# Kernel optimization log

Measured on AMD Instinct MI355X. Metric: run time of the kernel, lower is better.

The kernel has to match this reference:

```python
import jax, jax.numpy as jnp
import numpy as np

BN_EPS = 1e-5

def _bn_relu(x, gamma, beta):
    # training-mode BatchNorm1d: biased batch stats over (B, N) per channel
    mean = x.mean(axis=(0, 2), keepdims=True)
    var = x.var(axis=(0, 2), keepdims=True)
    xn = (x - mean) * jax.lax.rsqrt(var + BN_EPS)
    return jax.nn.relu(xn * gamma[None, :, None] + beta[None, :, None])


def setup_inputs() -> dict:
    key = jax.random.key(0)
    ks = jax.random.split(key, 12)
    B, n1, n2, c1, c2 = 16, 4096, 1024, 128, 256
    in_ch, mlp = c1 + c2, [256, 128]
    xyz1 = jax.random.uniform(ks[0], (B, n1, 3), dtype=jnp.float32)
    xyz2 = jax.random.uniform(ks[1], (B, n2, 3), dtype=jnp.float32)
    feat1 = jax.random.normal(ks[2], (B, c1, n1), dtype=jnp.float32)
    feat2 = jax.random.normal(ks[3], (B, c2, n2), dtype=jnp.float32)
    # Conv1d(k=1) weights as (out, in) matrices; kaiming-ish scale
    w0 = jax.random.normal(ks[4], (mlp[0], in_ch), dtype=jnp.float32) / np.sqrt(in_ch)
    b0 = jnp.zeros((mlp[0],), jnp.float32)
    g0 = jnp.ones((mlp[0],), jnp.float32)
    be0 = jnp.zeros((mlp[0],), jnp.float32)
    w1 = jax.random.normal(ks[5], (mlp[1], mlp[0]), dtype=jnp.float32) / np.sqrt(mlp[0])
    b1 = jnp.zeros((mlp[1],), jnp.float32)
    g1 = jnp.ones((mlp[1],), jnp.float32)
    be1 = jnp.zeros((mlp[1],), jnp.float32)
    return {"xyz1": xyz1, "xyz2": xyz2, "feat1": feat1, "feat2": feat2,
            "w0": w0, "b0": b0, "g0": g0, "be0": be0,
            "w1": w1, "b1": b1, "g1": g1, "be1": be1}


def reference(xyz1, xyz2, feat1, feat2, w0, b0, g0, be0, w1, b1, g1, be1):
    # three_nn_interpolate: squared pairwise dists (B, n1, n2)
    d = jnp.sum((xyz1[:, :, None, :] - xyz2[:, None, :, :]) ** 2, axis=-1)
    neg_d3, idx3 = jax.lax.top_k(-d, 3)          # 3 smallest dists
    d3 = -neg_d3                                  # (B, n1, 3)
    w = 1.0 / (d3 + 1e-8)
    w = w / jnp.sum(w, axis=-1, keepdims=True)
    # gather feat2 at knn indices: (B, c2, n1, 3)
    gathered = jnp.take_along_axis(feat2[:, :, None, :], idx3[:, None, :, :], axis=3)
    interp = jnp.sum(gathered * w[:, None, :, :], axis=-1)  # (B, c2, n1)

    x = jnp.concatenate([feat1, interp], axis=1)            # (B, c1+c2, n1)
    x = _bn_relu(jnp.einsum('oc,bcn->bon', w0, x) + b0[None, :, None], g0, be0)
    x = _bn_relu(jnp.einsum('oc,bcn->bon', w1, x) + b1[None, :, None], g1, be1)
    return x
```

## Files before the change

kernel.cpp:

```cpp
#include <hip/hip_runtime.h>
#include <hip/hip_bf16.h>

typedef unsigned short u16;
typedef __attribute__((ext_vector_type(8))) __bf16 bf16x8;
typedef __attribute__((ext_vector_type(4))) float floatx4;

#define B_   16
#define N1_  4096
#define N2_  1024
#define C1_  128
#define C2_  256
#define CIN_ 384
#define CM_  256
#define CO_  128

__device__ __forceinline__ u16 f2bf(float f) {
  unsigned u = __float_as_uint(f);
  u = (u + 0x7fffu + ((u >> 16) & 1u)) >> 16;
  return (u16)u;
}
__device__ __forceinline__ float bf2f(u16 h) {
  return __uint_as_float(((unsigned)h) << 16);
}

union U128 { uint4 u; bf16x8 v; u16 s[8]; };

__device__ __forceinline__ bf16x8 ldfrag(const u16* p) {
  U128 x; x.u = *(const uint4*)p; return x.v;
}
__device__ __forceinline__ uint4 pack8(const u16* h) {
  uint4 u;
  u.x = (unsigned)h[0] | ((unsigned)h[1] << 16);
  u.y = (unsigned)h[2] | ((unsigned)h[3] << 16);
  u.z = (unsigned)h[4] | ((unsigned)h[5] << 16);
  u.w = (unsigned)h[6] | ((unsigned)h[7] << 16);
  return u;
}


__global__ __launch_bounds__(256) void knn_part_kernel(
    const float* __restrict__ xyz1, const float* __restrict__ xyz2,
    float* __restrict__ pd, int* __restrict__ pi,
    const float* __restrict__ w0, const float* __restrict__ w1,
    u16* __restrict__ w0b, u16* __restrict__ w1b)
{
  __shared__ float4 sp[128];
  int t = threadIdx.x;
  if (blockIdx.x == 16) {
    int item = (blockIdx.y * 8 + blockIdx.z) * 256 + t;
    if (item < 12288) {
      int m = item / 48, kc = item % 48;
      const float* p = w0 + m * CIN_ + kc * 8;
      u16 h8[8];
      #pragma unroll
      for (int j = 0; j < 8; ++j) h8[j] = f2bf(p[j]);
      int mt = m >> 4, col = m & 15, kt = kc >> 2, quad = kc & 3;
      *(uint4*)(w0b + ((mt*12 + kt)*512 + (quad*16 + col)*8)) = pack8(h8);
    } else if (item < 16384) {
      int i2 = item - 12288;
      int m = i2 >> 5, kc = i2 & 31;
      const float* p = w1 + m * CM_ + kc * 8;
      u16 h8[8];
      #pragma unroll
      for (int j = 0; j < 8; ++j) h8[j] = f2bf(p[j]);
      int mt = m >> 4, col = m & 15, kt = kc >> 2, quad = kc & 3;
      *(uint4*)(w1b + ((mt*8 + kt)*512 + (quad*16 + col)*8)) = pack8(h8);
    }
    return;
  }
  int b = blockIdx.y, chunk = blockIdx.z;
  const float* p2 = xyz2 + ((size_t)b * N2_ + chunk * 128) * 3;
  if (t < 128) sp[t] = make_float4(p2[t*3], p2[t*3+1], p2[t*3+2], 0.f);
  __syncthreads();
  int i = blockIdx.x * 256 + t;
  const float* p1 = xyz1 + ((size_t)b * N1_ + i) * 3;
  float x = p1[0], y = p1[1], z = p1[2];
  float d0 = 1e30f, d1 = 1e30f, d2 = 1e30f;
  int i0 = 0, i1 = 0, i2 = 0;
  int jb = chunk * 128;
  #pragma unroll 4
  for (int j = 0; j < 128; ++j) {
    float4 p = sp[j];
    float dx = x - p.x, dy = y - p.y, dz = z - p.z;
    float d = dx*dx + dy*dy + dz*dz;
    int jj = jb + j;
    bool c2 = d < d2, c1 = d < d1, c0 = d < d0;
    d2 = c1 ? d1 : (c2 ? d  : d2);
    i2 = c1 ? i1 : (c2 ? jj : i2);
    d1 = c0 ? d0 : (c1 ? d  : d1);
    i1 = c0 ? i0 : (c1 ? jj : i1);
    d0 = c0 ? d  : d0;
    i0 = c0 ? jj : i0;
  }
  int o = chunk*65536 + b*4096 + i;
  pd[o] = d0; pd[o + 524288] = d1; pd[o + 1048576] = d2;
  pi[o] = i0; pi[o + 524288] = i1; pi[o + 1048576] = i2;
}

__global__ __launch_bounds__(256) void knn_merge_kernel(
    const float* __restrict__ pd, const int* __restrict__ pi,
    int* __restrict__ idx_out, float* __restrict__ w_out)
{
  int p = blockIdx.x * 256 + threadIdx.x;
  float d0 = 1e30f, d1 = 1e30f, d2 = 1e30f;
  int i0 = 0, i1 = 0, i2 = 0;
  #pragma unroll
  for (int c = 0; c < 8; ++c) {
    int o = c*65536 + p;
    #pragma unroll
    for (int k = 0; k < 3; ++k) {
      float d = pd[o + k*524288];
      int ix = pi[o + k*524288];
      bool c2 = d < d2, c1 = d < d1, c0 = d < d0;
      d2 = c1 ? d1 : (c2 ? d  : d2);
      i2 = c1 ? i1 : (c2 ? ix : i2);
      d1 = c0 ? d0 : (c1 ? d  : d1);
      i1 = c0 ? i0 : (c1 ? ix : i1);
      d0 = c0 ? d  : d0;
      i0 = c0 ? ix : i0;
    }
  }
  float w0 = 1.f/(d0+1e-8f), w1 = 1.f/(d1+1e-8f), w2 = 1.f/(d2+1e-8f);
  float inv = 1.f/(w0+w1+w2);
  idx_out[p]          = i0;
  idx_out[p +  65536] = i1;
  idx_out[p + 131072] = i2;
  w_out[p]            = w0*inv;
  w_out[p +  65536]   = w1*inv;
  w_out[p + 131072]   = w2*inv;
}

__global__ __launch_bounds__(256) void tr2_kernel(
    const float* __restrict__ feat2, u16* __restrict__ feat2Tb)
{
  __shared__ float sA[64][257];
  int b = blockIdx.y;
  int n0 = blockIdx.x * 64;
  int t = threadIdx.x;
  #pragma unroll
  for (int j = 0; j < 16; ++j) {
    int flat4 = t + j * 256;
    int c = flat4 >> 4, nn4 = (flat4 & 15) * 4;
    float4 v = *(const float4*)(feat2 + ((size_t)b*C2_ + c)*N2_ + n0 + nn4);
    sA[nn4+0][c] = v.x; sA[nn4+1][c] = v.y; sA[nn4+2][c] = v.z; sA[nn4+3][c] = v.w;
  }
  __syncthreads();
  int nn = t & 63, chunk = t >> 6;
  u16* dst = feat2Tb + ((size_t)b*N2_ + n0 + nn)*C2_ + chunk*64;
  #pragma unroll
  for (int g = 0; g < 8; ++g) {
    u16 h8[8];
    #pragma unroll
    for (int j = 0; j < 8; ++j) h8[j] = f2bf(sA[nn][chunk*64 + g*8 + j]);
    *(uint4*)(dst + g*8) = pack8(h8);
  }
}

__global__ __launch_bounds__(256) void prep_fused_kernel(
    const float* __restrict__ feat1, const u16* __restrict__ feat2Tb,
    const int* __restrict__ idx_in, const float* __restrict__ w_in,
    u16* __restrict__ xcatT)
{
  __shared__ float sA[64][133];
  int b = blockIdx.y;
  int t = threadIdx.x;
  if (blockIdx.x < 64) {
    int n0 = blockIdx.x * 64;
    #pragma unroll
    for (int j = 0; j < 8; ++j) {
      int flat4 = t + j * 256;
      int c = flat4 >> 4, nn4 = (flat4 & 15) * 4;
      float4 v = *(const float4*)(feat1 + ((size_t)b*C1_ + c)*N1_ + n0 + nn4);
      sA[nn4+0][c] = v.x; sA[nn4+1][c] = v.y; sA[nn4+2][c] = v.z; sA[nn4+3][c] = v.w;
    }
    __syncthreads();
    int nn = t & 63, chunk = t >> 6;
    int n = n0 + nn, nt = n >> 4, col = n & 15;
    u16* tb = xcatT + ((size_t)b*256 + nt)*12*512;
    #pragma unroll
    for (int g = 0; g < 4; ++g) {
      int c0 = chunk*32 + g*8;
      u16 h8[8];
      #pragma unroll
      for (int j = 0; j < 8; ++j) h8[j] = f2bf(sA[nn][c0 + j]);
      *(uint4*)(tb + (size_t)chunk*512 + (g*16 + col)*8) = pack8(h8);
    }
  } else {
    int p0 = (blockIdx.x - 64) * 64;
    int seg = t & 31;
    int pl  = t >> 5;
    #pragma unroll 2
    for (int pass = 0; pass < 8; ++pass) {
      int n = p0 + pass*8 + pl;
      int base = b*N1_ + n;
      int i0 = idx_in[base], i1 = idx_in[base + 65536], i2 = idx_in[base + 131072];
      float w0 = w_in[base], w1 = w_in[base + 65536], w2 = w_in[base + 131072];
      const u16* fb = feat2Tb + (size_t)b*N2_*C2_ + seg*8;
      U128 a, c, d;
      a.u = *(const uint4*)(fb + (size_t)i0*C2_);
      c.u = *(const uint4*)(fb + (size_t)i1*C2_);
      d.u = *(const uint4*)(fb + (size_t)i2*C2_);
      u16 h8[8];
      #pragma unroll
      for (int j = 0; j < 8; ++j)
        h8[j] = f2bf(w0*bf2f(a.s[j]) + w1*bf2f(c.s[j]) + w2*bf2f(d.s[j]));
      int nt = n >> 4, col = n & 15;
      int kt = 4 + (seg >> 2), quad = seg & 3;
      *(uint4*)(xcatT + (((size_t)b*256 + nt)*12 + kt)*512 + (quad*16 + col)*8) = pack8(h8);
    }
  }
}

__global__ __launch_bounds__(256) void gemm1_mfma(
    const u16* __restrict__ xcatT, const u16* __restrict__ w0b,
    const float* __restrict__ b0p, u16* __restrict__ y0T,
    float* __restrict__ p0)
{
  __shared__ u16 sbuf[2][16][512];
  __shared__ float ps[4][64][2];
  int t = threadIdx.x;
  int wave = t >> 6, lane = t & 63;
  int col = lane & 15, quad = lane >> 4;
  int wm = wave >> 1, wn = wave & 1;
  int b = blockIdx.y;
  int mtb8 = blockIdx.z * 8;
  int ntb8 = blockIdx.x * 8;

  const u16* asrc = w0b + (size_t)mtb8 * 12 * 512 + lane * 8;
  const u16* bsrc = xcatT + ((size_t)(b * 256 + ntb8) * 12) * 512 + lane * 8;
  const u16* stage_base = (wave < 2) ? (asrc + (size_t)(wave * 4) * 12 * 512)
                                     : (bsrc + (size_t)((wave - 2) * 4) * 12 * 512);

  floatx4 acc[4][4] = {};

  #pragma unroll
  for (int i = 0; i < 4; ++i)
    __builtin_amdgcn_global_load_lds(
        (const __attribute__((address_space(1))) void*)(stage_base + (size_t)i * 12 * 512),
        (__attribute__((address_space(3))) void*)(&sbuf[0][wave * 4 + i][0]),
        16, 0, 0);
  __syncthreads();

  int cur = 0;
  #pragma unroll 1
  for (int kt = 0; kt < 12; ++kt) {
    if (kt < 11) {
      #pragma unroll
      for (int i = 0; i < 4; ++i)
        __builtin_amdgcn_global_load_lds(
            (const __attribute__((address_space(1))) void*)(stage_base + (size_t)(i * 12 + kt + 1) * 512),
            (__attribute__((address_space(3))) void*)(&sbuf[cur ^ 1][wave * 4 + i][0]),
            16, 0, 0);
    }
    bf16x8 af[4], bfr[4];
    #pragma unroll
    for (int i = 0; i < 4; ++i) {
      af[i]  = ldfrag(&sbuf[cur][wm * 4 + i][lane * 8]);
      bfr[i] = ldfrag(&sbuf[cur][8 + wn * 4 + i][lane * 8]);
    }
    #pragma unroll
    for (int mt = 0; mt < 4; ++mt)
      #pragma unroll
      for (int nt = 0; nt < 4; ++nt)
        acc[mt][nt] = __builtin_amdgcn_mfma_f32_16x16x32_bf16(af[mt], bfr[nt], acc[mt][nt], 0, 0, 0);
    __syncthreads();
    cur ^= 1;
  }

  int m0 = blockIdx.z*128 + wm*64;
  #pragma unroll
  for (int mt = 0; mt < 4; ++mt) {
    float4 bias4 = *(const float4*)(b0p + m0 + mt*16 + quad*4);
    float bia[4] = {bias4.x, bias4.y, bias4.z, bias4.w};
    int kt_out = (m0 >> 5) + (mt >> 1);
    int quad_out = ((mt & 1) << 1) | (quad >> 1);
    int j0 = (quad & 1) * 4;
    float s[4] = {}, q[4] = {};
    int ntb = ntb8 + wn*4;
    #pragma unroll
    for (int nt = 0; nt < 4; ++nt) {
      int nt_g = ntb + nt;
      u16 h[4];
      #pragma unroll
      for (int r = 0; r < 4; ++r) {
        float v = acc[mt][nt][r] + bia[r];
        u16 hh = f2bf(v);
        float vr = bf2f(hh);
        h[r] = hh; s[r] += vr; q[r] += vr*vr;
      }
      *(ushort4*)(y0T + (((size_t)b*256 + nt_g)*8 + kt_out)*512 + (quad_out*16 + col)*8 + j0)
          = make_ushort4(h[0], h[1], h[2], h[3]);
    }
    #pragma unroll
    for (int r = 0; r < 4; ++r) {
      float ss = s[r], qq = q[r];
      #pragma unroll
      for (int msk = 1; msk < 16; msk <<= 1) { ss += __shfl_xor(ss, msk); qq += __shfl_xor(qq, msk); }
      if (col == 0) {
        ps[wave][mt*16 + quad*4 + r][0] = ss;
        ps[wave][mt*16 + quad*4 + r][1] = qq;
      }
    }
  }
  __syncthreads();
  {
    int c = t >> 1, k = t & 1;
    int wbase = (c >> 6) * 2, ch = c & 63;
    float v = ps[wbase][ch][k] + ps[wbase+1][ch][k];
    size_t l = (size_t)blockIdx.z*512 + blockIdx.y*32 + blockIdx.x;
    p0[l*256 + t] = v;
  }
}

__global__ __launch_bounds__(256) void stats_kernel(
    const float* __restrict__ p, const float* __restrict__ g,
    const float* __restrict__ be, float* __restrict__ scale,
    float* __restrict__ shift, int half_split)
{
  int c = blockIdx.x, t = threadIdx.x;
  size_t base = half_split ? ((size_t)(c >> 7) * 512 * 256 + (size_t)(c & 127) * 2)
                           : ((size_t)c * 2);
  float s = 0.f, q = 0.f;
  #pragma unroll
  for (int i = 0; i < 2; ++i) {
    float2 v = *(const float2*)(p + base + (size_t)(t + i*256) * 256);
    s += v.x; q += v.y;
  }
  #pragma unroll
  for (int m = 1; m < 64; m <<= 1) { s += __shfl_xor(s, m); q += __shfl_xor(q, m); }
  __shared__ float2 red[4];
  if ((t & 63) == 0) red[t >> 6] = make_float2(s, q);
  __syncthreads();
  if (t == 0) {
    float ss = red[0].x + red[1].x + red[2].x + red[3].x;
    float qq = red[0].y + red[1].y + red[2].y + red[3].y;
    float mu  = ss * (1.f/65536.f);
    float var = qq * (1.f/65536.f) - mu*mu;
    float a = g[c] * rsqrtf(var + 1e-5f);
    scale[c] = a; shift[c] = be[c] - mu*a;
  }
}

__global__ __launch_bounds__(256) void gemm2_mfma(
    const u16* __restrict__ y0T, const u16* __restrict__ w1b,
    const float* __restrict__ b1p,
    const float* __restrict__ scale0, const float* __restrict__ shift0,
    float* __restrict__ out, float* __restrict__ p1)
{
  __shared__ float a0s[CM_], bb0s[CM_];
  __shared__ float ps[4][64][2];
  int t = threadIdx.x;
  a0s[t] = scale0[t]; bb0s[t] = shift0[t];
  __syncthreads();
  int wave = t >> 6, lane = t & 63;
  int col = lane & 15, quad = lane >> 4;
  int wm = wave >> 1, wn = wave & 1;
  int b = blockIdx.y;
  int mtb = wm*4;
  int ntb = blockIdx.x*8 + wn*4;

  const u16* ap = w1b + lane*8;
  const u16* bp = y0T + ((size_t)(b*256 + ntb)*8)*512 + lane*8;

  floatx4 acc[4][4] = {};
  bf16x8 af[4], afn[4];
  U128 braw[4], brawn[4];
  #pragma unroll
  for (int i = 0; i < 4; ++i) {
    af[i] = ldfrag(ap + (size_t)((mtb+i)*8)*512);
    braw[i].u = *(const uint4*)(bp + (size_t)(i*8)*512);
  }
  #pragma unroll 1
  for (int kt = 1; kt < 8; ++kt) {
    #pragma unroll
    for (int i = 0; i < 4; ++i) afn[i] = ldfrag(ap + (size_t)((mtb+i)*8 + kt)*512);
    #pragma unroll
    for (int i = 0; i < 4; ++i) brawn[i].u = *(const uint4*)(bp + (size_t)(i*8 + kt)*512);
    int c0 = (kt-1)*32 + quad*8;
    float4 av0 = *(const float4*)&a0s[c0], av1 = *(const float4*)&a0s[c0+4];
    float4 bv0 = *(const float4*)&bb0s[c0], bv1 = *(const float4*)&bb0s[c0+4];
    float av[8] = {av0.x,av0.y,av0.z,av0.w,av1.x,av1.y,av1.z,av1.w};
    float bv[8] = {bv0.x,bv0.y,bv0.z,bv0.w,bv1.x,bv1.y,bv1.z,bv1.w};
    bf16x8 bfv[4];
    #pragma unroll
    for (int i = 0; i < 4; ++i) {
      u16 h8[8];
      #pragma unroll
      for (int j = 0; j < 8; ++j)
        h8[j] = f2bf(fmaxf(fmaf(bf2f(braw[i].s[j]), av[j], bv[j]), 0.f));
      U128 x; x.u = pack8(h8); bfv[i] = x.v;
    }
    #pragma unroll
    for (int mt = 0; mt < 4; ++mt)
      #pragma unroll
      for (int nt = 0; nt < 4; ++nt)
        acc[mt][nt] = __builtin_amdgcn_mfma_f32_16x16x32_bf16(af[mt], bfv[nt], acc[mt][nt], 0, 0, 0);
    #pragma unroll
    for (int i = 0; i < 4; ++i) { af[i] = afn[i]; braw[i] = brawn[i]; }
  }
  {
    int c0 = 7*32 + quad*8;
    float4 av0 = *(const float4*)&a0s[c0], av1 = *(const float4*)&a0s[c0+4];
    float4 bv0 = *(const float4*)&bb0s[c0], bv1 = *(const float4*)&bb0s[c0+4];
    float av[8] = {av0.x,av0.y,av0.z,av0.w,av1.x,av1.y,av1.z,av1.w};
    float bv[8] = {bv0.x,bv0.y,bv0.z,bv0.w,bv1.x,bv1.y,bv1.z,bv1.w};
    bf16x8 bfv[4];
    #pragma unroll
    for (int i = 0; i < 4; ++i) {
      u16 h8[8];
      #pragma unroll
      for (int j = 0; j < 8; ++j)
        h8[j] = f2bf(fmaxf(fmaf(bf2f(braw[i].s[j]), av[j], bv[j]), 0.f));
      U128 x; x.u = pack8(h8); bfv[i] = x.v;
    }
    #pragma unroll
    for (int mt = 0; mt < 4; ++mt)
      #pragma unroll
      for (int nt = 0; nt < 4; ++nt)
        acc[mt][nt] = __builtin_amdgcn_mfma_f32_16x16x32_bf16(af[mt], bfv[nt], acc[mt][nt], 0, 0, 0);
  }

  int m0 = wm*64;
  int n0 = blockIdx.x*128 + wn*64;
  #pragma unroll
  for (int mt = 0; mt < 4; ++mt) {
    float4 bias4 = *(const float4*)(b1p + m0 + mt*16 + quad*4);
    float bia[4] = {bias4.x, bias4.y, bias4.z, bias4.w};
    float s[4] = {}, q[4] = {};
    #pragma unroll
    for (int nt = 0; nt < 4; ++nt) {
      int n = n0 + nt*16 + col;
      #pragma unroll
      for (int r = 0; r < 4; ++r) {
        float v = acc[mt][nt][r] + bia[r];
        out[((size_t)b*CO_ + m0 + mt*16 + quad*4 + r)*N1_ + n] = v;
        s[r] += v; q[r] += v*v;
      }
    }
    #pragma unroll
    for (int r = 0; r < 4; ++r) {
      float ss = s[r], qq = q[r];
      #pragma unroll
      for (int msk = 1; msk < 16; msk <<= 1) { ss += __shfl_xor(ss, msk); qq += __shfl_xor(qq, msk); }
      if (col == 0) {
        ps[wave][mt*16 + quad*4 + r][0] = ss;
        ps[wave][mt*16 + quad*4 + r][1] = qq;
      }
    }
  }
  __syncthreads();
  {
    int c = t >> 1, k = t & 1;
    int wbase = (c >> 6) * 2, ch = c & 63;
    float v = ps[wbase][ch][k] + ps[wbase+1][ch][k];
    size_t l = (size_t)blockIdx.y*32 + blockIdx.x;
    p1[l*256 + t] = v;
  }
}

__global__ __launch_bounds__(256) void bnrelu_kernel(
    float* __restrict__ out, const float* __restrict__ scale1, const float* __restrict__ shift1)
{
  int idx = blockIdx.x * 256 + threadIdx.x;
  int c = (idx >> 10) & (CO_ - 1);
  float a = scale1[c];
  float bb = shift1[c];
  float4 v = ((const float4*)out)[idx];
  v.x = fmaxf(fmaf(v.x, a, bb), 0.f);
  v.y = fmaxf(fmaf(v.y, a, bb), 0.f);
  v.z = fmaxf(fmaf(v.z, a, bb), 0.f);
  v.w = fmaxf(fmaf(v.w, a, bb), 0.f);
  ((float4*)out)[idx] = v;
}

extern "C" void kernel_launch(void* const* d_in, const int* in_sizes, int n_in,
                              void* d_out, int out_size, void* d_ws, size_t ws_size,
                              hipStream_t stream)
{
  const float* xyz1  = (const float*)d_in[0];
  const float* xyz2  = (const float*)d_in[1];
  const float* feat1 = (const float*)d_in[2];
  const float* feat2 = (const float*)d_in[3];
  const float* w0    = (const float*)d_in[4];
  const float* b0    = (const float*)d_in[5];
  const float* g0    = (const float*)d_in[6];
  const float* be0   = (const float*)d_in[7];
  const float* w1    = (const float*)d_in[8];
  const float* b1    = (const float*)d_in[9];
  const float* g1    = (const float*)d_in[10];
  const float* be1   = (const float*)d_in[11];
  float* out = (float*)d_out;
  char* ws = (char*)d_ws;

  u16*   xcatT   = (u16*)ws;
  float* knn_pd  = (float*)ws;
  int*   knn_pi  = (int*)(ws + 6291456);
  u16*   y0T     = (u16*)(ws + 50331648);
  u16*   feat2Tb = (u16*)(ws + 50331648);
  u16*   w0b     = (u16*)(ws + 83886080);
  u16*   w1b     = (u16*)(ws + 84082688);
  int*   idx_buf = (int*)(ws + 84148224);
  float* w_buf   = (float*)(ws + 84934656);
  float* p0      = (float*)(ws + 85721088);
  float* p1      = (float*)(ws + 86769664);
  float* scale0  = (float*)(ws + 87293952);
  float* shift0  = scale0 + 256;
  float* scale1  = scale0 + 512;
  float* shift1  = scale0 + 640;

  knn_part_kernel <<<dim3(17,16,8),   256, 0, stream>>>(xyz1, xyz2, knn_pd, knn_pi, w0, w1, w0b, w1b);
  knn_merge_kernel<<<256,             256, 0, stream>>>(knn_pd, knn_pi, idx_buf, w_buf);
  tr2_kernel      <<<dim3(16,16),     256, 0, stream>>>(feat2, feat2Tb);
  prep_fused_kernel<<<dim3(128,16),   256, 0, stream>>>(feat1, feat2Tb, idx_buf, w_buf, xcatT);
  gemm1_mfma      <<<dim3(32,16,2),   256, 0, stream>>>(xcatT, w0b, b0, y0T, p0);
  stats_kernel    <<<256,             256, 0, stream>>>(p0, g0, be0, scale0, shift0, 1);
  gemm2_mfma      <<<dim3(32,16),     256, 0, stream>>>(y0T, w1b, b1, scale0, shift0, out, p1);
  stats_kernel    <<<128,             256, 0, stream>>>(p1, g1, be1, scale1, shift1, 0);
  bnrelu_kernel   <<<8192,            256, 0, stream>>>(out, scale1, shift1);
}
```

Before: 244.7 us.

## Fuse kNN merge with feat2 transpose, branch top-3 insert, LDS-staged gemm2

The kNN inner loop now uses an early-out branch, so the top-3 insertion only runs when a candidate beats the current third-best. The merge and feat2 transpose kernels become one launch that splits blocks by blockIdx.x, saving a launch. gemm2 is rewritten to stage weight and activation fragments into double-buffered LDS with global_load_lds, using smaller 64-column tiles and twice as many blocks for occupancy. The stats kernel takes a loop count to match, and the p1 partials move into the reused workspace region at offset 0.

```diff
diff --git a/kernel.cpp b/kernel.cpp
--- a/kernel.cpp
+++ b/kernel.cpp
@@ -83,60 +83,57 @@
     float4 p = sp[j];
     float dx = x - p.x, dy = y - p.y, dz = z - p.z;
     float d = dx*dx + dy*dy + dz*dz;
-    int jj = jb + j;
-    bool c2 = d < d2, c1 = d < d1, c0 = d < d0;
-    d2 = c1 ? d1 : (c2 ? d  : d2);
-    i2 = c1 ? i1 : (c2 ? jj : i2);
-    d1 = c0 ? d0 : (c1 ? d  : d1);
-    i1 = c0 ? i0 : (c1 ? jj : i1);
-    d0 = c0 ? d  : d0;
-    i0 = c0 ? jj : i0;
+    if (d < d2) {
+      int jj = jb + j;
+      if (d < d0)      { d2=d1; i2=i1; d1=d0; i1=i0; d0=d; i0=jj; }
+      else if (d < d1) { d2=d1; i2=i1; d1=d;  i1=jj; }
+      else             { d2=d;  i2=jj; }
+    }
   }
   int o = chunk*65536 + b*4096 + i;
   pd[o] = d0; pd[o + 524288] = d1; pd[o + 1048576] = d2;
   pi[o] = i0; pi[o + 524288] = i1; pi[o + 1048576] = i2;
 }
 
-__global__ __launch_bounds__(256) void knn_merge_kernel(
+__global__ __launch_bounds__(256) void tr2m_kernel(
+    const float* __restrict__ feat2, u16* __restrict__ feat2Tb,
     const float* __restrict__ pd, const int* __restrict__ pi,
     int* __restrict__ idx_out, float* __restrict__ w_out)
 {
-  int p = blockIdx.x * 256 + threadIdx.x;
-  float d0 = 1e30f, d1 = 1e30f, d2 = 1e30f;
-  int i0 = 0, i1 = 0, i2 = 0;
-  #pragma unroll
-  for (int c = 0; c < 8; ++c) {
-    int o = c*65536 + p;
-    #pragma unroll
-    for (int k = 0; k < 3; ++k) {
-      float d = pd[o + k*524288];
-      int ix = pi[o + k*524288];
-      bool c2 = d < d2, c1 = d < d1, c0 = d < d0;
-      d2 = c1 ? d1 : (c2 ? d  : d2);
-      i2 = c1 ? i1 : (c2 ? ix : i2);
-      d1 = c0 ? d0 : (c1 ? d  : d1);
-      i1 = c0 ? i0 : (c1 ? ix : i1);
-      d0 = c0 ? d  : d0;
-      i0 = c0 ? ix : i0;
-    }
-  }
-  float w0 = 1.f/(d0+1e-8f), w1 = 1.f/(d1+1e-8f), w2 = 1.f/(d2+1e-8f);
-  float inv = 1.f/(w0+w1+w2);
-  idx_out[p]          = i0;
-  idx_out[p +  65536] = i1;
-  idx_out[p + 131072] = i2;
-  w_out[p]            = w0*inv;
-  w_out[p +  65536]   = w1*inv;
-  w_out[p + 131072]   = w2*inv;
-}
-
-__global__ __launch_bounds__(256) void tr2_kernel(
-    const float* __restrict__ feat2, u16* __restrict__ feat2Tb)
-{
   __shared__ float sA[64][257];
+  int t = threadIdx.x;
+  if (blockIdx.x >= 16) {
+    int p = (blockIdx.y * 16 + (blockIdx.x - 16)) * 256 + t;
+    float d0 = 1e30f, d1 = 1e30f, d2 = 1e30f;
+    int i0 = 0, i1 = 0, i2 = 0;
+    #pragma unroll
+    for (int c = 0; c < 8; ++c) {
+      int o = c*65536 + p;
+      #pragma unroll
+      for (int k = 0; k < 3; ++k) {
+        float d = pd[o + k*524288];
+        int ix = pi[o + k*524288];
+        bool c2 = d < d2, c1 = d < d1, c0 = d < d0;
+        d2 = c1 ? d1 : (c2 ? d  : d2);
+        i2 = c1 ? i1 : (c2 ? ix : i2);
+        d1 = c0 ? d0 : (c1 ? d  : d1);
+        i1 = c0 ? i0 : (c1 ? ix : i1);
+        d0 = c0 ? d  : d0;
+        i0 = c0 ? ix : i0;
+      }
+    }
+    float w0 = 1.f/(d0+1e-8f), w1 = 1.f/(d1+1e-8f), w2 = 1.f/(d2+1e-8f);
+    float inv = 1.f/(w0+w1+w2);
+    idx_out[p]          = i0;
+    idx_out[p +  65536] = i1;
+    idx_out[p + 131072] = i2;
+    w_out[p]            = w0*inv;
+    w_out[p +  65536]   = w1*inv;
+    w_out[p + 131072]   = w2*inv;
+    return;
+  }
   int b = blockIdx.y;
   int n0 = blockIdx.x * 64;
-  int t = threadIdx.x;
   #pragma unroll
   for (int j = 0; j < 16; ++j) {
     int flat4 = t + j * 256;
@@ -315,14 +312,13 @@
 __global__ __launch_bounds__(256) void stats_kernel(
     const float* __restrict__ p, const float* __restrict__ g,
     const float* __restrict__ be, float* __restrict__ scale,
-    float* __restrict__ shift, int half_split)
+    float* __restrict__ shift, int half_split, int nl)
 {
   int c = blockIdx.x, t = threadIdx.x;
   size_t base = half_split ? ((size_t)(c >> 7) * 512 * 256 + (size_t)(c & 127) * 2)
                            : ((size_t)c * 2);
   float s = 0.f, q = 0.f;
-  #pragma unroll
-  for (int i = 0; i < 2; ++i) {
+  for (int i = 0; i < nl; ++i) {
     float2 v = *(const float2*)(p + base + (size_t)(t + i*256) * 256);
     s += v.x; q += v.y;
   }
@@ -347,88 +343,82 @@
     const float* __restrict__ scale0, const float* __restrict__ shift0,
     float* __restrict__ out, float* __restrict__ p1)
 {
+  __shared__ u16 sbuf[2][12][512];
   __shared__ float a0s[CM_], bb0s[CM_];
   __shared__ float ps[4][64][2];
   int t = threadIdx.x;
   a0s[t] = scale0[t]; bb0s[t] = shift0[t];
-  __syncthreads();
   int wave = t >> 6, lane = t & 63;
   int col = lane & 15, quad = lane >> 4;
   int wm = wave >> 1, wn = wave & 1;
   int b = blockIdx.y;
-  int mtb = wm*4;
-  int ntb = blockIdx.x*8 + wn*4;
-
-  const u16* ap = w1b + lane*8;
-  const u16* bp = y0T + ((size_t)(b*256 + ntb)*8)*512 + lane*8;
-
-  floatx4 acc[4][4] = {};
-  bf16x8 af[4], afn[4];
-  U128 braw[4], brawn[4];
-  #pragma unroll
-  for (int i = 0; i < 4; ++i) {
-    af[i] = ldfrag(ap + (size_t)((mtb+i)*8)*512);
-    braw[i].u = *(const uint4*)(bp + (size_t)(i*8)*512);
-  }
+  int ntb4 = blockIdx.x * 4;
+
+  const u16* src[3];
+  #pragma unroll
+  for (int i = 0; i < 3; ++i) {
+    int f = wave * 3 + i;
+    src[i] = (f < 8) ? (w1b + (size_t)(f * 8) * 512 + lane * 8)
+                     : (y0T + ((size_t)(b * 256 + ntb4 + (f - 8)) * 8) * 512 + lane * 8);
+  }
+
+  floatx4 acc[4][2] = {};
+
+  #pragma unroll
+  for (int i = 0; i < 3; ++i)
+    __builtin_amdgcn_global_load_lds(
+        (const __attribute__((address_space(1))) void*)(src[i]),
+        (__attribute__((address_space(3))) void*)(&sbuf[0][wave * 3 + i][0]),
+        16, 0, 0);
+  __syncthreads();
+
+  int cur = 0;
   #pragma unroll 1
-  for (int kt = 1; kt < 8; ++kt) {
-    #pragma unroll
-    for (int i = 0; i < 4; ++i) afn[i] = ldfrag(ap + (size_t)((mtb+i)*8 + kt)*512);
-    #pragma unroll
-    for (int i = 0; i < 4; ++i) brawn[i].u = *(const uint4*)(bp + (size_t)(i*8 + kt)*512);
-    int c0 = (kt-1)*32 + quad*8;
-    float4 av0 = *(const float4*)&a0s[c0], av1 = *(const float4*)&a0s[c0+4];
-    float4 bv0 = *(const float4*)&bb0s[c0], bv1 = *(const float4*)&bb0s[c0+4];
-    float av[8] = {av0.x,av0.y,av0.z,av0.w,av1.x,av1.y,av1.z,av1.w};
-    float bv[8] = {bv0.x,bv0.y,bv0.z,bv0.w,bv1.x,bv1.y,bv1.z,bv1.w};
-    bf16x8 bfv[4];
-    #pragma unroll
-    for (int i = 0; i < 4; ++i) {
+  for (int kt = 0; kt < 8; ++kt) {
+    if (kt < 7) {
+      #pragma unroll
+      for (int i = 0; i < 3; ++i)
+        __builtin_amdgcn_global_load_lds(
+            (const __attribute__((address_space(1))) void*)(src[i] + (size_t)(kt + 1) * 512),
+            (__attribute__((address_space(3))) void*)(&sbuf[cur ^ 1][wave * 3 + i][0]),
+            16, 0, 0);
+    }
+    bf16x8 af[4]; U128 braw[2];
+    #pragma unroll
+    for (int i = 0; i < 4; ++i) af[i] = ldfrag(&sbuf[cur][wm * 4 + i][lane * 8]);
+    #pragma unroll
+    for (int j = 0; j < 2; ++j) braw[j].u = *(const uint4*)(&sbuf[cur][8 + wn * 2 + j][lane * 8]);
+    int c0 = kt * 32 + quad * 8;
+    float av[8], bv[8];
+    *(float4*)&av[0] = *(const float4*)&a0s[c0];  *(float4*)&av[4] = *(const float4*)&a0s[c0+4];
+    *(float4*)&bv[0] = *(const float4*)&bb0s[c0]; *(float4*)&bv[4] = *(const float4*)&bb0s[c0+4];
+    bf16x8 bfv[2];
+    #pragma unroll
+    for (int j = 0; j < 2; ++j) {
       u16 h8[8];
       #pragma unroll
-      for (int j = 0; j < 8; ++j)
-        h8[j] = f2bf(fmaxf(fmaf(bf2f(braw[i].s[j]), av[j], bv[j]), 0.f));
-      U128 x; x.u = pack8(h8); bfv[i] = x.v;
+      for (int e = 0; e < 8; ++e)
+        h8[e] = f2bf(fmaxf(fmaf(bf2f(braw[j].s[e]), av[e], bv[e]), 0.f));
+      U128 x; x.u = pack8(h8); bfv[j] = x.v;
     }
     #pragma unroll
     for (int mt = 0; mt < 4; ++mt)
       #pragma unroll
-      for (int nt = 0; nt < 4; ++nt)
+      for (int nt = 0; nt < 2; ++nt)
         acc[mt][nt] = __builtin_amdgcn_mfma_f32_16x16x32_bf16(af[mt], bfv[nt], acc[mt][nt], 0, 0, 0);
-    #pragma unroll
-    for (int i = 0; i < 4; ++i) { af[i] = afn[i]; braw[i] = brawn[i]; }
-  }
-  {
-    int c0 = 7*32 + quad*8;
-    float4 av0 = *(const float4*)&a0s[c0], av1 = *(const float4*)&a0s[c0+4];
-    float4 bv0 = *(const float4*)&bb0s[c0], bv1 = *(const float4*)&bb0s[c0+4];
-    float av[8] = {av0.x,av0.y,av0.z,av0.w,av1.x,av1.y,av1.z,av1.w};
-    float bv[8] = {bv0.x,bv0.y,bv0.z,bv0.w,bv1.x,bv1.y,bv1.z,bv1.w};
-    bf16x8 bfv[4];
-    #pragma unroll
-    for (int i = 0; i < 4; ++i) {
-      u16 h8[8];
-      #pragma unroll
-      for (int j = 0; j < 8; ++j)
-        h8[j] = f2bf(fmaxf(fmaf(bf2f(braw[i].s[j]), av[j], bv[j]), 0.f));
-      U128 x; x.u = pack8(h8); bfv[i] = x.v;
-    }
-    #pragma unroll
-    for (int mt = 0; mt < 4; ++mt)
-      #pragma unroll
-      for (int nt = 0; nt < 4; ++nt)
-        acc[mt][nt] = __builtin_amdgcn_mfma_f32_16x16x32_bf16(af[mt], bfv[nt], acc[mt][nt], 0, 0, 0);
-  }
-
-  int m0 = wm*64;
-  int n0 = blockIdx.x*128 + wn*64;
+    __syncthreads();
+    cur ^= 1;
+  }
+
+  int m0 = wm * 64;
+  int n0 = blockIdx.x * 64 + wn * 32;
   #pragma unroll
   for (int mt = 0; mt < 4; ++mt) {
     float4 bias4 = *(const float4*)(b1p + m0 + mt*16 + quad*4);
     float bia[4] = {bias4.x, bias4.y, bias4.z, bias4.w};
     float s[4] = {}, q[4] = {};
     #pragma unroll
-    for (int nt = 0; nt < 4; ++nt) {
+    for (int nt = 0; nt < 2; ++nt) {
       int n = n0 + nt*16 + col;
       #pragma unroll
       for (int r = 0; r < 4; ++r) {
@@ -453,7 +443,7 @@
     int c = t >> 1, k = t & 1;
     int wbase = (c >> 6) * 2, ch = c & 63;
     float v = ps[wbase][ch][k] + ps[wbase+1][ch][k];
-    size_t l = (size_t)blockIdx.y*32 + blockIdx.x;
+    size_t l = (size_t)blockIdx.y*64 + blockIdx.x;
     p1[l*256 + t] = v;
   }
 }
@@ -494,6 +484,7 @@
 
   u16*   xcatT   = (u16*)ws;
   float* knn_pd  = (float*)ws;
+  float* p1      = (float*)ws;
   int*   knn_pi  = (int*)(ws + 6291456);
   u16*   y0T     = (u16*)(ws + 50331648);
   u16*   feat2Tb = (u16*)(ws + 50331648);
@@ -502,19 +493,17 @@
   int*   idx_buf = (int*)(ws + 84148224);
   float* w_buf   = (float*)(ws + 84934656);
   float* p0      = (float*)(ws + 85721088);
-  float* p1      = (float*)(ws + 86769664);
   float* scale0  = (float*)(ws + 87293952);
   float* shift0  = scale0 + 256;
   float* scale1  = scale0 + 512;
   float* shift1  = scale0 + 640;
 
   knn_part_kernel <<<dim3(17,16,8),   256, 0, stream>>>(xyz1, xyz2, knn_pd, knn_pi, w0, w1, w0b, w1b);
-  knn_merge_kernel<<<256,             256, 0, stream>>>(knn_pd, knn_pi, idx_buf, w_buf);
-  tr2_kernel      <<<dim3(16,16),     256, 0, stream>>>(feat2, feat2Tb);
+  tr2m_kernel     <<<dim3(32,16),     256, 0, stream>>>(feat2, feat2Tb, knn_pd, knn_pi, idx_buf, w_buf);
   prep_fused_kernel<<<dim3(128,16),   256, 0, stream>>>(feat1, feat2Tb, idx_buf, w_buf, xcatT);
   gemm1_mfma      <<<dim3(32,16,2),   256, 0, stream>>>(xcatT, w0b, b0, y0T, p0);
-  stats_kernel    <<<256,             256, 0, stream>>>(p0, g0, be0, scale0, shift0, 1);
-  gemm2_mfma      <<<dim3(32,16),     256, 0, stream>>>(y0T, w1b, b1, scale0, shift0, out, p1);
-  stats_kernel    <<<128,             256, 0, stream>>>(p1, g1, be1, scale1, shift1, 0);
+  stats_kernel    <<<256,             256, 0, stream>>>(p0, g0, be0, scale0, shift0, 1, 2);
+  gemm2_mfma      <<<dim3(64,16),     256, 0, stream>>>(y0T, w1b, b1, scale0, shift0, out, p1);
+  stats_kernel    <<<128,             256, 0, stream>>>(p1, g1, be1, scale1, shift1, 0, 4);
   bnrelu_kernel   <<<8192,            256, 0, stream>>>(out, scale1, shift1);
 }
```

Measured after the change: 244.4 us. About the same (-0.1%).
